# Optimization experiments

Measured on AMD Instinct MI355X. Metric: run time of the kernel, lower is better.

## Reference

```python
import jax, jax.numpy as jnp
import numpy as np
import math

B, S, IN, D, H, L, DFF = 8, 512, 32, 512, 8, 6, 2048
DK = D // H
LN_EPS = 1e-5
KL_EPS = 1e-8


def _pos_encoding(seq_len, d_model):
    pe = np.zeros((seq_len, d_model), dtype=np.float32)
    pos = np.arange(seq_len, dtype=np.float32)[:, None]
    div = np.exp(np.arange(0, d_model, 2, dtype=np.float32) * (-math.log(10000.0) / d_model))
    pe[:, 0::2] = np.sin(pos * div)
    pe[:, 1::2] = np.cos(pos * div)
    return jnp.asarray(pe)


def setup_inputs() -> dict:
    key = jax.random.key(0)
    ks = iter(jax.random.split(key, 32))
    g = lambda shape: jax.random.normal(next(ks), shape, dtype=jnp.float32) * 0.02
    return {
        'x': jax.random.normal(next(ks), (B, S, IN), dtype=jnp.float32),
        'W_in': g((IN, D)), 'b_in': jnp.zeros((D,), jnp.float32),
        'pe': _pos_encoding(S, D),
        'Wq': g((L, D, D)), 'Wk': g((L, D, D)), 'Wv': g((L, D, D)),
        'Wo': g((L, D, D)), 'bo': jnp.zeros((L, D), jnp.float32),
        'W1': g((L, D, DFF)), 'b1': jnp.zeros((L, DFF), jnp.float32),
        'W2': g((L, DFF, D)), 'b2': jnp.zeros((L, D), jnp.float32),
        'ln1_g': jnp.ones((L, D), jnp.float32), 'ln1_b': jnp.zeros((L, D), jnp.float32),
        'ln2_g': jnp.ones((L, D), jnp.float32), 'ln2_b': jnp.zeros((L, D), jnp.float32),
        'W_out': g((D, IN)), 'b_out': jnp.zeros((IN,), jnp.float32),
        'Ws1': g((D, D // 2)), 'bs1': jnp.zeros((D // 2,), jnp.float32),
        'Ws2': g((D // 2, 1)), 'bs2': jnp.zeros((1,), jnp.float32),
    }


def _layernorm(v, gamma, beta):
    mu = v.mean(-1, keepdims=True)
    var = ((v - mu) ** 2).mean(-1, keepdims=True)
    return (v - mu) * jax.lax.rsqrt(var + LN_EPS) * gamma + beta


def reference(x, W_in, b_in, pe, Wq, Wk, Wv, Wo, bo, W1, b1, W2, b2,
              ln1_g, ln1_b, ln2_g, ln2_b, W_out, b_out, Ws1, bs1, Ws2, bs2):
    b, s, _ = x.shape
    h = x @ W_in + b_in + pe[None, :s, :]
    total_assoc = jnp.zeros((b, s), x.dtype)
    scale = 1.0 / math.sqrt(DK)
    prior = 1.0 / s + KL_EPS
    for l in range(L):
        # QKV: [b, h, s, dk]
        Q = (h @ Wq[l]).reshape(b, s, H, DK).transpose(0, 2, 1, 3)
        K = (h @ Wk[l]).reshape(b, s, H, DK).transpose(0, 2, 1, 3)
        V = (h @ Wv[l]).reshape(b, s, H, DK).transpose(0, 2, 1, 3)
        scores = jnp.einsum('bhsk,bhtk->bhst', Q, K) * scale
        attn = jax.nn.softmax(scores, axis=-1)  # [b,h,s,s]
        ctx = jnp.einsum('bhst,bhtk->bhsk', attn, V)
        ctx = ctx.transpose(0, 2, 1, 3).reshape(b, s, D)
        attn_out = ctx @ Wo[l] + bo[l]
        # association discrepancy: KL(avg_attn || uniform prior) per query
        avg_attn = attn.mean(axis=1) + KL_EPS  # [b,s,s]
        total_assoc = total_assoc + (avg_attn * jnp.log(avg_attn / prior)).sum(-1)
        h = _layernorm(h + attn_out, ln1_g[l], ln1_b[l])
        ff = jax.nn.relu(h @ W1[l] + b1[l]) @ W2[l] + b2[l]
        h = _layernorm(h + ff, ln2_g[l], ln2_b[l])
    reconstruction = h @ W_out + b_out
    anomaly_scores = jax.nn.sigmoid(jax.nn.relu(h @ Ws1 + bs1) @ Ws2 + bs2)[..., 0]
    avg_association = total_assoc / L
    return reconstruction, anomaly_scores, avg_association
```

## Files before the change

### kernel.cpp

```cpp
#include <hip/hip_runtime.h>
#include <math.h>

typedef __attribute__((ext_vector_type(8))) short bf16x8;
typedef __attribute__((ext_vector_type(4))) float f32x4;

__device__ __forceinline__ short f2bf(float v) {
  union { float f; unsigned u; } x; x.f = v;
  unsigned r = x.u + 0x7fffu + ((x.u >> 16) & 1u);
  return (short)(r >> 16);
}

__device__ __forceinline__ float bf2f(unsigned short u) {
  union { unsigned u; float f; } x; x.u = ((unsigned)u) << 16;
  return x.f;
}

__device__ __forceinline__ void gld_lds16(const void* g, void* l) {
  __builtin_amdgcn_global_load_lds((const __attribute__((address_space(1))) void*)g,
                                   (__attribute__((address_space(3))) void*)l, 16, 0, 0);
}

__global__ __launch_bounds__(256) void prologue_kernel(
    const float* __restrict__ x, const float* __restrict__ W_in, const float* __restrict__ b_in,
    const float* __restrict__ pe, short* __restrict__ hbf,
    const float* __restrict__ Wq, const float* __restrict__ Wk, const float* __restrict__ Wv,
    const float* __restrict__ Wo, const float* __restrict__ W1, const float* __restrict__ W2,
    const float* __restrict__ Ws1, const float* __restrict__ Wout,
    short* __restrict__ qkvt, short* __restrict__ wot, short* __restrict__ w1t,
    short* __restrict__ w2t, short* __restrict__ ws1t, short* __restrict__ woutT) {
  __shared__ float t[32][33];
  const int tid = threadIdx.x;
  int idx = blockIdx.x;
  if (idx < 8192) {
    int col = (idx & 1) * 256 + tid;
    int row = idx >> 1;
    int s = row & 511;
    float a = b_in[col] + pe[s * 512 + col];
    const float* xr = x + (size_t)row * 32;
#pragma unroll
    for (int k = 0; k < 32; k++) a += xr[k] * W_in[k * 512 + col];
    hbf[(size_t)row * 512 + col] = f2bf(a);
    return;
  }
  idx -= 8192;
  const float* src;
  short* dst;
  int R, C, cx, cy;
  if (idx < 4608) {
    int z = idx >> 8, rem = idx & 255;
    cx = rem & 15; cy = rem >> 4;
    int which = z / 6, l = z % 6;
    src = (which == 0 ? Wq : which == 1 ? Wk : Wv) + (size_t)l * 262144;
    dst = qkvt + (size_t)l * 786432 + (size_t)which * 262144;
    R = 512; C = 512;
  } else if (idx < 6144) {
    int j = idx - 4608;
    int l = j >> 8, rem = j & 255;
    cx = rem & 15; cy = rem >> 4;
    src = Wo + (size_t)l * 262144; dst = wot + (size_t)l * 262144;
    R = 512; C = 512;
  } else if (idx < 12288) {
    int j = idx - 6144;
    int l = j >> 10, rem = j & 1023;
    cx = rem & 63; cy = rem >> 6;
    src = W1 + (size_t)l * 1048576; dst = w1t + (size_t)l * 1048576;
    R = 512; C = 2048;
  } else if (idx < 18432) {
    int j = idx - 12288;
    int l = j >> 10, rem = j & 1023;
    cx = rem & 15; cy = rem >> 4;
    src = W2 + (size_t)l * 1048576; dst = w2t + (size_t)l * 1048576;
    R = 2048; C = 512;
  } else if (idx < 18560) {
    int j = idx - 18432;
    cx = j & 7; cy = j >> 3;
    src = Ws1; dst = ws1t; R = 512; C = 256;
  } else {
    int j = idx - 18560;
    cx = 0; cy = j;
    src = Wout; dst = woutT; R = 512; C = 32;
  }
  const int tx = tid & 31, ty = tid >> 5;
  const int c0 = cx * 32, r0 = cy * 32;
#pragma unroll
  for (int i = 0; i < 4; i++)
    t[ty + i * 8][tx] = src[(size_t)(r0 + ty + i * 8) * C + c0 + tx];
  __syncthreads();
#pragma unroll
  for (int i = 0; i < 4; i++)
    dst[(size_t)(c0 + ty + i * 8) * R + r0 + tx] = f2bf(t[tx][ty + i * 8]);
}

template <int EPI, int BM, int BN, int BK>
__global__ __launch_bounds__(256) void gemm_bt(const short* __restrict__ A,
                                               const short* __restrict__ Bt,
                                               short* __restrict__ Cb,
                                               const float* __restrict__ bias,
                                               int M, int N, int K) {
  __shared__ short As[BM * BK];
  __shared__ short Bs[BN * BK];
  const int tid = threadIdx.x;
  const int wid = tid >> 6;
  const int lane = tid & 63;
  const int m0 = blockIdx.y * BM;
  const int n0 = blockIdx.x * BN;
  constexpr int WR = BM / 2, WC = BN / 2, FI = WR / 16, FJ = WC / 16, KK = BK / 32;
  const int wr = (wid >> 1) * WR;
  const int wc = (wid & 1) * WC;

  f32x4 acc[FI][FJ];
#pragma unroll
  for (int i = 0; i < FI; i++)
#pragma unroll
    for (int j = 0; j < FJ; j++)
#pragma unroll
      for (int q = 0; q < 4; q++) acc[i][j][q] = 0.0f;

  const short* aBase = A + (size_t)m0 * K;
  const short* bBase = Bt + (size_t)n0 * K;
  constexpr int RPC = 512 / BK;
  constexpr int CA = BM / RPC;
  constexpr int CT = (BM + BN) / RPC;
  const int rowL = lane / (64 / RPC);
  const int colE = (lane % (64 / RPC)) * 8;
  const int kg = (lane >> 4) * 8;
  const int r16 = lane & 15;

  for (int kt = 0; kt < K; kt += BK) {
    __syncthreads();
#pragma unroll
    for (int c = 0; c < CT / 4; ++c) {
      int s = c * 4 + wid;
      if (s < CA)
        gld_lds16(aBase + (size_t)(s * RPC + rowL) * K + kt + colE, As + s * 512);
      else
        gld_lds16(bBase + (size_t)((s - CA) * RPC + rowL) * K + kt + colE, Bs + (s - CA) * 512);
    }
    __syncthreads();
    bf16x8 af[FI][KK], bfr[FJ][KK];
#pragma unroll
    for (int i = 0; i < FI; i++)
#pragma unroll
      for (int kk = 0; kk < KK; kk++)
        af[i][kk] = *(const bf16x8*)&As[(wr + i * 16 + r16) * BK + kk * 32 + kg];
#pragma unroll
    for (int j = 0; j < FJ; j++)
#pragma unroll
      for (int kk = 0; kk < KK; kk++)
        bfr[j][kk] = *(const bf16x8*)&Bs[(wc + j * 16 + r16) * BK + kk * 32 + kg];
#pragma unroll
    for (int kk = 0; kk < KK; kk++)
#pragma unroll
      for (int i = 0; i < FI; i++)
#pragma unroll
        for (int j = 0; j < FJ; j++)
          acc[i][j] = __builtin_amdgcn_mfma_f32_16x16x32_bf16(af[i][kk], bfr[j][kk], acc[i][j], 0, 0, 0);
  }

  const int col16 = lane & 15;
  const int rowg = (lane >> 4) * 4;
#pragma unroll
  for (int i = 0; i < FI; i++) {
    int row = m0 + wr + i * 16 + rowg;
#pragma unroll
    for (int j = 0; j < FJ; j++) {
      int col = n0 + wc + j * 16 + col16;
      float bv = (EPI == 2 || EPI == 4) ? bias[col] : 0.0f;
#pragma unroll
      for (int q = 0; q < 4; q++) {
        float v = acc[i][j][q] + bv;
        if (EPI == 2) {
          v = fmaxf(v, 0.0f);
          Cb[(size_t)(row + q) * N + col] = f2bf(v);
        } else if (EPI == 5) {
          int rr = row + q;
          int sect = col >> 9, hh = (col >> 6) & 7, dk = col & 63;
          int bq = rr >> 9, tt = rr & 511;
          Cb[(((size_t)(sect * 64 + bq * 8 + hh)) * 512 + tt) * 64 + dk] = f2bf(v);
        } else {
          Cb[(size_t)(row + q) * N + col] = f2bf(v);
        }
      }
    }
  }
}

__global__ __launch_bounds__(256) void vt_kernel(const short* __restrict__ qh,
                                                 short* __restrict__ Vt) {
  __shared__ short t[32][34];
  const int bh = blockIdx.z;
  const int t0 = blockIdx.x * 32, d0 = blockIdx.y * 32;
  const int tx = threadIdx.x & 31, ty = threadIdx.x >> 5;
  const short* Vh = qh + (size_t)(128 + bh) * 512 * 64;
#pragma unroll
  for (int i = 0; i < 4; i++)
    t[ty + i * 8][tx] = Vh[(size_t)(t0 + ty + i * 8) * 64 + d0 + tx];
  __syncthreads();
#pragma unroll
  for (int i = 0; i < 4; i++)
    Vt[((size_t)bh * 64 + d0 + ty + i * 8) * 512 + t0 + tx] = t[tx][ty + i * 8];
}

__global__ __launch_bounds__(256) void smpv_kernel(const short* __restrict__ qh,
                                                   const short* __restrict__ Vt,
                                                   short* __restrict__ P,
                                                   short* __restrict__ ctxb) {
  __shared__ short Pl[16 * 512];
  __shared__ float red0[4][16];
  __shared__ float red1[4][16];
  const int bh = blockIdx.y, b = bh >> 3, h = bh & 7;
  const int q0 = blockIdx.x * 16;
  const int tid = threadIdx.x;
  const int wid = tid >> 6, lane = tid & 63;
  const int r16 = lane & 15, g = lane >> 4;

  const short* Qh = qh + ((size_t)bh * 512) * 64;
  const short* Kh = qh + ((size_t)(64 + bh) * 512) * 64;

  const short* qp = Qh + (size_t)(q0 + r16) * 64 + g * 8;
  const bf16x8 qa0 = *(const bf16x8*)qp;
  const bf16x8 qa1 = *(const bf16x8*)(qp + 32);

  f32x4 acc[8];
#pragma unroll
  for (int tt = 0; tt < 8; ++tt) {
    const short* kp = Kh + (size_t)(wid * 128 + tt * 16 + r16) * 64 + g * 8;
    bf16x8 kb0 = *(const bf16x8*)kp;
    bf16x8 kb1 = *(const bf16x8*)(kp + 32);
    f32x4 c = {0.f, 0.f, 0.f, 0.f};
    c = __builtin_amdgcn_mfma_f32_16x16x32_bf16(qa0, kb0, c, 0, 0, 0);
    c = __builtin_amdgcn_mfma_f32_16x16x32_bf16(qa1, kb1, c, 0, 0, 0);
    acc[tt] = c;
  }

  float mx[4] = {-1e30f, -1e30f, -1e30f, -1e30f};
#pragma unroll
  for (int tt = 0; tt < 8; ++tt)
#pragma unroll
    for (int r = 0; r < 4; ++r) mx[r] = fmaxf(mx[r], acc[tt][r]);
#pragma unroll
  for (int r = 0; r < 4; ++r)
#pragma unroll
    for (int m = 8; m; m >>= 1) mx[r] = fmaxf(mx[r], __shfl_xor(mx[r], m, 16));
  if (r16 == 0) {
#pragma unroll
    for (int r = 0; r < 4; ++r) red0[wid][g * 4 + r] = mx[r];
  }
  __syncthreads();
#pragma unroll
  for (int r = 0; r < 4; ++r) {
    int q = g * 4 + r;
    mx[r] = fmaxf(fmaxf(red0[0][q], red0[1][q]), fmaxf(red0[2][q], red0[3][q]));
  }
  float sum[4] = {0.f, 0.f, 0.f, 0.f};
#pragma unroll
  for (int tt = 0; tt < 8; ++tt)
#pragma unroll
    for (int r = 0; r < 4; ++r) {
      float e = __expf((acc[tt][r] - mx[r]) * 0.125f);
      acc[tt][r] = e;
      sum[r] += e;
    }
#pragma unroll
  for (int r = 0; r < 4; ++r)
#pragma unroll
    for (int m = 8; m; m >>= 1) sum[r] += __shfl_xor(sum[r], m, 16);
  if (r16 == 0) {
#pragma unroll
    for (int r = 0; r < 4; ++r) red1[wid][g * 4 + r] = sum[r];
  }
  __syncthreads();

  char* plc = (char*)Pl;
#pragma unroll
  for (int r = 0; r < 4; ++r) {
    int q = g * 4 + r;
    float inv = 1.0f / (red1[0][q] + red1[1][q] + red1[2][q] + red1[3][q]);
    int swz = (q & 7) << 4;
#pragma unroll
    for (int tt = 0; tt < 8; ++tt)
      *(short*)(plc + q * 1024 + (((wid * 128 + tt * 16 + r16) * 2) ^ swz)) =
          f2bf(acc[tt][r] * inv);
  }
  __syncthreads();

  short* pg = P + ((size_t)bh * 512 + q0) * 512;
#pragma unroll
  for (int k = 0; k < 4; ++k) {
    int c = k * 256 + tid;
    int q = c >> 6;
    int tB = (c & 63) * 16;
    bf16x8 v = *(const bf16x8*)(plc + q * 1024 + (tB ^ ((q & 7) << 4)));
    *(bf16x8*)&pg[(size_t)q * 512 + (c & 63) * 8] = v;
  }

  f32x4 pacc = {0.f, 0.f, 0.f, 0.f};
  const short* vb = Vt + (size_t)bh * 64 * 512 + (size_t)(wid * 16) * 512;
  const int rswz = (r16 & 7) << 4;
  for (int kt = 0; kt < 512; kt += 32) {
    bf16x8 af = *(const bf16x8*)(plc + r16 * 1024 + (((kt + g * 8) * 2) ^ rswz));
    bf16x8 bfr = *(const bf16x8*)&vb[(size_t)r16 * 512 + kt + g * 8];
    pacc = __builtin_amdgcn_mfma_f32_16x16x32_bf16(af, bfr, pacc, 0, 0, 0);
  }
  const int col = h * 64 + wid * 16 + r16;
#pragma unroll
  for (int q = 0; q < 4; ++q)
    ctxb[(size_t)(b * 512 + q0 + g * 4 + q) * 512 + col] = f2bf(pacc[q]);
}

template <int FIRST>
__global__ __launch_bounds__(256) void wo_kl_kernel(const short* __restrict__ A,
                                                    const short* __restrict__ Bt,
                                                    const float* __restrict__ bias,
                                                    short* __restrict__ aout,
                                                    const short* __restrict__ P,
                                                    float* __restrict__ assoc) {
  __shared__ short As[64 * 32];
  __shared__ short Bs[64 * 32];
  const int tid = threadIdx.x;
  const int wid = tid >> 6, lane = tid & 63;
  if (blockIdx.x < 8) {
    const int m0 = blockIdx.y * 64;
    const int n0 = blockIdx.x * 64;
    const int wr = (wid >> 1) * 32;
    const int wc = (wid & 1) * 32;
    f32x4 acc[2][2];
#pragma unroll
    for (int i = 0; i < 2; i++)
#pragma unroll
      for (int j = 0; j < 2; j++)
#pragma unroll
        for (int q = 0; q < 4; q++) acc[i][j][q] = 0.0f;
    const short* aBase = A + (size_t)m0 * 512;
    const short* bBase = Bt + (size_t)n0 * 512;
    const int rowL = lane >> 2;
    const int colE = (lane & 3) * 8;
    const int kg = (lane >> 4) * 8;
    const int r16 = lane & 15;
    for (int kt = 0; kt < 512; kt += 32) {
      __syncthreads();
#pragma unroll
      for (int c = 0; c < 2; ++c) {
        int s = c * 4 + wid;
        if (s < 4)
          gld_lds16(aBase + (size_t)(s * 16 + rowL) * 512 + kt + colE, As + s * 512);
        else
          gld_lds16(bBase + (size_t)((s - 4) * 16 + rowL) * 512 + kt + colE, Bs + (s - 4) * 512);
      }
      __syncthreads();
      bf16x8 af[2], bfr[2];
#pragma unroll
      for (int i = 0; i < 2; i++)
        af[i] = *(const bf16x8*)&As[(wr + i * 16 + r16) * 32 + kg];
#pragma unroll
      for (int j = 0; j < 2; j++)
        bfr[j] = *(const bf16x8*)&Bs[(wc + j * 16 + r16) * 32 + kg];
#pragma unroll
      for (int i = 0; i < 2; i++)
#pragma unroll
        for (int j = 0; j < 2; j++)
          acc[i][j] = __builtin_amdgcn_mfma_f32_16x16x32_bf16(af[i], bfr[j], acc[i][j], 0, 0, 0);
    }
    const int col16 = lane & 15;
    const int rowg = (lane >> 4) * 4;
#pragma unroll
    for (int i = 0; i < 2; i++) {
      int row = m0 + wr + i * 16 + rowg;
#pragma unroll
      for (int j = 0; j < 2; j++) {
        int col = n0 + wc + j * 16 + col16;
        float bv = bias[col];
#pragma unroll
        for (int q = 0; q < 4; q++)
          aout[(size_t)(row + q) * 512 + col] = f2bf(acc[i][j][q] + bv);
      }
    }
  } else {
    const int kb = (blockIdx.x - 8) * 64 + blockIdx.y;
    const int row = kb * 4 + wid;
    const int b = row >> 9, q = row & 511;
    const float prior = 1.0f / 512.0f + 1e-8f;
    float hs[8] = {0.f, 0.f, 0.f, 0.f, 0.f, 0.f, 0.f, 0.f};
#pragma unroll
    for (int h = 0; h < 8; ++h) {
      bf16x8 v = *(const bf16x8*)&P[(((size_t)(b * 8 + h)) * 512 + q) * 512 + lane * 8];
#pragma unroll
      for (int k = 0; k < 8; ++k) hs[k] += bf2f((unsigned short)v[k]);
    }
    float s = 0.f;
#pragma unroll
    for (int k = 0; k < 8; ++k) {
      float a = hs[k] * 0.125f + 1e-8f;
      s += a * __logf(a / prior);
    }
#pragma unroll
    for (int m = 32; m; m >>= 1) s += __shfl_xor(s, m, 64);
    if (lane == 0) assoc[row] = FIRST ? s : (assoc[row] + s);
  }
}

__global__ __launch_bounds__(256) void ln_kernel(const short* __restrict__ res,
                                                 const float* __restrict__ g,
                                                 const float* __restrict__ bta,
                                                 short* __restrict__ hbf) {
  const int wid = threadIdx.x >> 6, lane = threadIdx.x & 63;
  const size_t row = (size_t)blockIdx.x * 4 + wid;
  bf16x8 hv = *(const bf16x8*)&hbf[row * 512 + lane * 8];
  bf16x8 rv = *(const bf16x8*)&res[row * 512 + lane * 8];
  float v[8], s = 0.f, s2 = 0.f;
#pragma unroll
  for (int i = 0; i < 8; i++) {
    v[i] = bf2f((unsigned short)hv[i]) + bf2f((unsigned short)rv[i]);
    s += v[i];
    s2 += v[i] * v[i];
  }
#pragma unroll
  for (int m = 32; m; m >>= 1) {
    s += __shfl_xor(s, m, 64);
    s2 += __shfl_xor(s2, m, 64);
  }
  float mu = s * (1.0f / 512.0f);
  float var = s2 * (1.0f / 512.0f) - mu * mu;
  float rs = rsqrtf(var + 1e-5f);
  const float* gp = g + lane * 8;
  const float* bp = bta + lane * 8;
  bf16x8 ob;
#pragma unroll
  for (int i = 0; i < 8; i++) ob[i] = f2bf((v[i] - mu) * rs * gp[i] + bp[i]);
  *(bf16x8*)&hbf[row * 512 + lane * 8] = ob;
}

__global__ __launch_bounds__(256) void recon_mfma(const short* __restrict__ hbf,
                                                  const short* __restrict__ WoutT,
                                                  const float* __restrict__ bout,
                                                  float* __restrict__ out) {
  const int wid = threadIdx.x >> 6, lane = threadIdx.x & 63;
  const int r16 = lane & 15, kg = (lane >> 4) * 8;
  const int wbase = blockIdx.x * 128 + wid * 32;

  f32x4 acc[2][2];
#pragma unroll
  for (int i = 0; i < 2; i++)
#pragma unroll
    for (int j = 0; j < 2; j++)
#pragma unroll
      for (int q = 0; q < 4; q++) acc[i][j][q] = 0.0f;

  for (int kt = 0; kt < 512; kt += 32) {
    bf16x8 af[2], bfr[2];
#pragma unroll
    for (int i = 0; i < 2; i++)
      af[i] = *(const bf16x8*)&hbf[(size_t)(wbase + i * 16 + r16) * 512 + kt + kg];
#pragma unroll
    for (int j = 0; j < 2; j++)
      bfr[j] = *(const bf16x8*)&WoutT[(size_t)(j * 16 + r16) * 512 + kt + kg];
#pragma unroll
    for (int i = 0; i < 2; i++)
#pragma unroll
      for (int j = 0; j < 2; j++)
        acc[i][j] = __builtin_amdgcn_mfma_f32_16x16x32_bf16(af[i], bfr[j], acc[i][j], 0, 0, 0);
  }

  const int rowg = (lane >> 4) * 4;
#pragma unroll
  for (int i = 0; i < 2; i++)
#pragma unroll
    for (int j = 0; j < 2; j++) {
      int col = j * 16 + r16;
#pragma unroll
      for (int q = 0; q < 4; q++)
        out[(size_t)(wbase + i * 16 + rowg + q) * 32 + col] = acc[i][j][q] + bout[col];
    }
}

__global__ __launch_bounds__(256) void score2_kernel(const short* __restrict__ s1,
                                                     const float* __restrict__ Ws2,
                                                     const float* __restrict__ bs2,
                                                     const float* __restrict__ assoc,
                                                     float* __restrict__ outScore,
                                                     float* __restrict__ outAssoc) {
  const int wid = threadIdx.x >> 6, lane = threadIdx.x & 63;
  const int row = blockIdx.x * 4 + wid;
  const short* rp = &s1[(size_t)row * 256 + lane * 4];
  float d = 0.f;
#pragma unroll
  for (int e = 0; e < 4; e++) d += bf2f((unsigned short)rp[e]) * Ws2[lane * 4 + e];
#pragma unroll
  for (int m = 32; m; m >>= 1) d += __shfl_xor(d, m, 64);
  if (lane == 0) {
    outScore[row] = 1.f / (1.f + __expf(-(d + bs2[0])));
    outAssoc[row] = assoc[row] * (1.0f / 6.0f);
  }
}

extern "C" void kernel_launch(void* const* d_in, const int* in_sizes, int n_in,
                              void* d_out, int out_size, void* d_ws, size_t ws_size,
                              hipStream_t stream) {
  const float* x    = (const float*)d_in[0];
  const float* W_in = (const float*)d_in[1];
  const float* b_in = (const float*)d_in[2];
  const float* pe   = (const float*)d_in[3];
  const float* Wq   = (const float*)d_in[4];
  const float* Wk   = (const float*)d_in[5];
  const float* Wv   = (const float*)d_in[6];
  const float* Wo   = (const float*)d_in[7];
  const float* bo   = (const float*)d_in[8];
  const float* W1   = (const float*)d_in[9];
  const float* b1   = (const float*)d_in[10];
  const float* W2   = (const float*)d_in[11];
  const float* b2   = (const float*)d_in[12];
  const float* ln1g = (const float*)d_in[13];
  const float* ln1b = (const float*)d_in[14];
  const float* ln2g = (const float*)d_in[15];
  const float* ln2b = (const float*)d_in[16];
  const float* Wout = (const float*)d_in[17];
  const float* bout = (const float*)d_in[18];
  const float* Ws1  = (const float*)d_in[19];
  const float* bs1  = (const float*)d_in[20];
  const float* Ws2  = (const float*)d_in[21];
  const float* bs2  = (const float*)d_in[22];

  char* p = (char*)d_ws;
  auto alloc = [&](size_t bytes) {
    void* r = (void*)p;
    p += (bytes + 255) & ~(size_t)255;
    return r;
  };
  short* h_bf  = (short*)alloc((size_t)4096 * 512 * 2);
  short* qh    = (short*)alloc((size_t)4096 * 1536 * 2);
  short* aout  = (short*)alloc((size_t)4096 * 512 * 2);
  short* ctxb  = (short*)alloc((size_t)4096 * 512 * 2);
  short* ff1b  = (short*)alloc((size_t)4096 * 2048 * 2);
  short* ff2   = (short*)alloc((size_t)4096 * 512 * 2);
  float* assoc = (float*)alloc((size_t)4096 * 4);
  short* Pbuf  = (short*)alloc((size_t)64 * 512 * 512 * 2);
  short* Vt    = (short*)alloc((size_t)64 * 64 * 512 * 2);
  short* sc1   = (short*)alloc((size_t)4096 * 256 * 2);
  short* qkvt  = (short*)alloc((size_t)6 * 1536 * 512 * 2);
  short* wot   = (short*)alloc((size_t)6 * 512 * 512 * 2);
  short* w1t   = (short*)alloc((size_t)6 * 2048 * 512 * 2);
  short* w2t   = (short*)alloc((size_t)6 * 512 * 2048 * 2);
  short* ws1t  = (short*)alloc((size_t)256 * 512 * 2);
  short* woutT = (short*)alloc((size_t)32 * 512 * 2);

  prologue_kernel<<<26768, 256, 0, stream>>>(x, W_in, b_in, pe, h_bf, Wq, Wk, Wv, Wo, W1, W2,
                                             Ws1, Wout, qkvt, wot, w1t, w2t, ws1t, woutT);

  for (int l = 0; l < 6; ++l) {
    gemm_bt<5, 128, 128, 32><<<dim3(12, 32), 256, 0, stream>>>(
        h_bf, qkvt + (size_t)l * 786432, qh, nullptr, 4096, 1536, 512);
    vt_kernel<<<dim3(16, 2, 64), 256, 0, stream>>>(qh, Vt);
    smpv_kernel<<<dim3(32, 64), 256, 0, stream>>>(qh, Vt, Pbuf, ctxb);
    if (l == 0)
      wo_kl_kernel<1><<<dim3(24, 64), 256, 0, stream>>>(ctxb, wot + (size_t)l * 262144,
                                                        bo + l * 512, aout, Pbuf, assoc);
    else
      wo_kl_kernel<0><<<dim3(24, 64), 256, 0, stream>>>(ctxb, wot + (size_t)l * 262144,
                                                        bo + l * 512, aout, Pbuf, assoc);
    ln_kernel<<<1024, 256, 0, stream>>>(aout, ln1g + l * 512, ln1b + l * 512, h_bf);
    gemm_bt<2, 128, 128, 32><<<dim3(16, 32), 256, 0, stream>>>(
        h_bf, w1t + (size_t)l * 1048576, ff1b, b1 + l * 2048, 4096, 2048, 512);
    gemm_bt<4, 64, 64, 32><<<dim3(8, 64), 256, 0, stream>>>(
        ff1b, w2t + (size_t)l * 1048576, ff2, b2 + l * 512, 4096, 512, 2048);
    ln_kernel<<<1024, 256, 0, stream>>>(ff2, ln2g + l * 512, ln2b + l * 512, h_bf);
  }

  float* out = (float*)d_out;
  recon_mfma<<<32, 256, 0, stream>>>(h_bf, woutT, bout, out);
  gemm_bt<2, 128, 128, 32><<<dim3(2, 32), 256, 0, stream>>>(h_bf, ws1t, sc1, bs1,
                                                            4096, 256, 512);
  score2_kernel<<<1024, 256, 0, stream>>>(sc1, Ws2, bs2, assoc, out + 131072,
                                          out + 131072 + 4096);
}
```

Baseline: 798.0 us.

## Fuse V transpose into QKV GEMM epilogue, split PV accumulators, retile FF2

The QKV GEMM epilogue now writes V directly in transposed layout as packed 4-short stores, so the separate vt_kernel launch and its extra read and write of V are gone. The PV loop in smpv_kernel uses two independent MFMA accumulators to shorten the dependent MFMA chain. The FF2 GEMM tile changes from 64x64 to 128x64, halving the block count and raising per-block reuse. Risks are less coalesced transposed V stores and lower occupancy for FF2.

Result: slower. 834.1 us (+4.5%).

```diff
diff --git a/kernel.cpp b/kernel.cpp
--- a/kernel.cpp
+++ b/kernel.cpp
@@ -2,6 +2,7 @@
 #include <math.h>
 
 typedef __attribute__((ext_vector_type(8))) short bf16x8;
+typedef __attribute__((ext_vector_type(4))) short short4v;
 typedef __attribute__((ext_vector_type(4))) float f32x4;
 
 __device__ __forceinline__ short f2bf(float v) {
@@ -95,6 +96,7 @@
 __global__ __launch_bounds__(256) void gemm_bt(const short* __restrict__ A,
                                                const short* __restrict__ Bt,
                                                short* __restrict__ Cb,
+                                               short* __restrict__ Vt,
                                                const float* __restrict__ bias,
                                                int M, int N, int K) {
   __shared__ short As[BM * BK];
@@ -165,40 +167,31 @@
 #pragma unroll
     for (int j = 0; j < FJ; j++) {
       int col = n0 + wc + j * 16 + col16;
-      float bv = (EPI == 2 || EPI == 4) ? bias[col] : 0.0f;
-#pragma unroll
-      for (int q = 0; q < 4; q++) {
-        float v = acc[i][j][q] + bv;
-        if (EPI == 2) {
-          v = fmaxf(v, 0.0f);
-          Cb[(size_t)(row + q) * N + col] = f2bf(v);
-        } else if (EPI == 5) {
-          int rr = row + q;
-          int sect = col >> 9, hh = (col >> 6) & 7, dk = col & 63;
-          int bq = rr >> 9, tt = rr & 511;
-          Cb[(((size_t)(sect * 64 + bq * 8 + hh)) * 512 + tt) * 64 + dk] = f2bf(v);
+      if (EPI == 5) {
+        int sect = col >> 9, hh = (col >> 6) & 7, dk = col & 63;
+        int bq = row >> 9, tt = row & 511;
+        if (sect < 2) {
+#pragma unroll
+          for (int q = 0; q < 4; q++)
+            Cb[(((size_t)(sect * 64 + bq * 8 + hh)) * 512 + tt + q) * 64 + dk] =
+                f2bf(acc[i][j][q]);
         } else {
+          short4v pk;
+#pragma unroll
+          for (int q = 0; q < 4; q++) pk[q] = f2bf(acc[i][j][q]);
+          *(short4v*)&Vt[((size_t)(bq * 8 + hh) * 64 + dk) * 512 + tt] = pk;
+        }
+      } else {
+        float bv = bias[col];
+#pragma unroll
+        for (int q = 0; q < 4; q++) {
+          float v = acc[i][j][q] + bv;
+          if (EPI == 2) v = fmaxf(v, 0.0f);
           Cb[(size_t)(row + q) * N + col] = f2bf(v);
         }
       }
     }
   }
-}
-
-__global__ __launch_bounds__(256) void vt_kernel(const short* __restrict__ qh,
-                                                 short* __restrict__ Vt) {
-  __shared__ short t[32][34];
-  const int bh = blockIdx.z;
-  const int t0 = blockIdx.x * 32, d0 = blockIdx.y * 32;
-  const int tx = threadIdx.x & 31, ty = threadIdx.x >> 5;
-  const short* Vh = qh + (size_t)(128 + bh) * 512 * 64;
-#pragma unroll
-  for (int i = 0; i < 4; i++)
-    t[ty + i * 8][tx] = Vh[(size_t)(t0 + ty + i * 8) * 64 + d0 + tx];
-  __syncthreads();
-#pragma unroll
-  for (int i = 0; i < 4; i++)
-    Vt[((size_t)bh * 64 + d0 + ty + i * 8) * 512 + t0 + tx] = t[tx][ty + i * 8];
 }
 
 __global__ __launch_bounds__(256) void smpv_kernel(const short* __restrict__ qh,
@@ -294,18 +287,21 @@
     *(bf16x8*)&pg[(size_t)q * 512 + (c & 63) * 8] = v;
   }
 
-  f32x4 pacc = {0.f, 0.f, 0.f, 0.f};
+  f32x4 pacc0 = {0.f, 0.f, 0.f, 0.f}, pacc1 = {0.f, 0.f, 0.f, 0.f};
   const short* vb = Vt + (size_t)bh * 64 * 512 + (size_t)(wid * 16) * 512;
   const int rswz = (r16 & 7) << 4;
-  for (int kt = 0; kt < 512; kt += 32) {
-    bf16x8 af = *(const bf16x8*)(plc + r16 * 1024 + (((kt + g * 8) * 2) ^ rswz));
-    bf16x8 bfr = *(const bf16x8*)&vb[(size_t)r16 * 512 + kt + g * 8];
-    pacc = __builtin_amdgcn_mfma_f32_16x16x32_bf16(af, bfr, pacc, 0, 0, 0);
+  for (int kt = 0; kt < 512; kt += 64) {
+    bf16x8 af0 = *(const bf16x8*)(plc + r16 * 1024 + (((kt + g * 8) * 2) ^ rswz));
+    bf16x8 af1 = *(const bf16x8*)(plc + r16 * 1024 + (((kt + 32 + g * 8) * 2) ^ rswz));
+    bf16x8 b0 = *(const bf16x8*)&vb[(size_t)r16 * 512 + kt + g * 8];
+    bf16x8 b1 = *(const bf16x8*)&vb[(size_t)r16 * 512 + kt + 32 + g * 8];
+    pacc0 = __builtin_amdgcn_mfma_f32_16x16x32_bf16(af0, b0, pacc0, 0, 0, 0);
+    pacc1 = __builtin_amdgcn_mfma_f32_16x16x32_bf16(af1, b1, pacc1, 0, 0, 0);
   }
   const int col = h * 64 + wid * 16 + r16;
 #pragma unroll
   for (int q = 0; q < 4; ++q)
-    ctxb[(size_t)(b * 512 + q0 + g * 4 + q) * 512 + col] = f2bf(pacc[q]);
+    ctxb[(size_t)(b * 512 + q0 + g * 4 + q) * 512 + col] = f2bf(pacc0[q] + pacc1[q]);
 }
 
 template <int FIRST>
@@ -548,8 +544,7 @@
 
   for (int l = 0; l < 6; ++l) {
     gemm_bt<5, 128, 128, 32><<<dim3(12, 32), 256, 0, stream>>>(
-        h_bf, qkvt + (size_t)l * 786432, qh, nullptr, 4096, 1536, 512);
-    vt_kernel<<<dim3(16, 2, 64), 256, 0, stream>>>(qh, Vt);
+        h_bf, qkvt + (size_t)l * 786432, qh, Vt, nullptr, 4096, 1536, 512);
     smpv_kernel<<<dim3(32, 64), 256, 0, stream>>>(qh, Vt, Pbuf, ctxb);
     if (l == 0)
       wo_kl_kernel<1><<<dim3(24, 64), 256, 0, stream>>>(ctxb, wot + (size_t)l * 262144,
@@ -559,15 +554,15 @@
                                                         bo + l * 512, aout, Pbuf, assoc);
     ln_kernel<<<1024, 256, 0, stream>>>(aout, ln1g + l * 512, ln1b + l * 512, h_bf);
     gemm_bt<2, 128, 128, 32><<<dim3(16, 32), 256, 0, stream>>>(
-        h_bf, w1t + (size_t)l * 1048576, ff1b, b1 + l * 2048, 4096, 2048, 512);
-    gemm_bt<4, 64, 64, 32><<<dim3(8, 64), 256, 0, stream>>>(
-        ff1b, w2t + (size_t)l * 1048576, ff2, b2 + l * 512, 4096, 512, 2048);
+        h_bf, w1t + (size_t)l * 1048576, ff1b, nullptr, b1 + l * 2048, 4096, 2048, 512);
+    gemm_bt<4, 128, 64, 32><<<dim3(8, 32), 256, 0, stream>>>(
+        ff1b, w2t + (size_t)l * 1048576, ff2, nullptr, b2 + l * 512, 4096, 512, 2048);
     ln_kernel<<<1024, 256, 0, stream>>>(ff2, ln2g + l * 512, ln2b + l * 512, h_bf);
   }
 
   float* out = (float*)d_out;
   recon_mfma<<<32, 256, 0, stream>>>(h_bf, woutT, bout, out);
-  gemm_bt<2, 128, 128, 32><<<dim3(2, 32), 256, 0, stream>>>(h_bf, ws1t, sc1, bs1,
+  gemm_bt<2, 128, 128, 32><<<dim3(2, 32), 256, 0, stream>>>(h_bf, ws1t, sc1, nullptr, bs1,
                                                             4096, 256, 512);
   score2_kernel<<<1024, 256, 0, stream>>>(sc1, Ws2, bs2, assoc, out + 131072,
                                           out + 131072 + 4096);
```
